# Optimization experiments

Measured on AMD Instinct MI355X. Metric: run time of the kernel, lower is better.

## Reference

```python
import jax, jax.numpy as jnp
import numpy as np

N_NODES = 50000
N_EDGES = 800000
IN_C, HID_C, OUT_C = 128, 128, 64
N_GRAPHS = 64
NEG_SLOPE = 0.2


def setup_inputs() -> dict:
    key = jax.random.key(0)
    ks = jax.random.split(key, 16)
    x = jax.random.normal(ks[0], (N_NODES, IN_C), dtype=jnp.float32)
    edge_index = jax.random.randint(ks[1], (2, N_EDGES), 0, N_NODES, dtype=jnp.int64)
    batch = jnp.sort(jax.random.randint(ks[2], (N_NODES,), 0, N_GRAPHS, dtype=jnp.int64))
    dims = [(IN_C, HID_C), (HID_C, HID_C), (HID_C, OUT_C)]
    inp = {"x": x, "edge_index": edge_index, "batch": batch}
    for l, (din, dout) in enumerate(dims):
        s = 1.0 / np.sqrt(din)
        inp[f"W{l}"] = jax.random.normal(ks[3 + 4 * l], (din, dout), dtype=jnp.float32) * s
        inp[f"as{l}"] = jax.random.normal(ks[4 + 4 * l], (dout,), dtype=jnp.float32) * 0.1
        inp[f"ad{l}"] = jax.random.normal(ks[5 + 4 * l], (dout,), dtype=jnp.float32) * 0.1
        inp[f"b{l}"] = jnp.zeros((dout,), dtype=jnp.float32)
    return inp


def gat_conv(x, src, dst, W, a_src, a_dst, b, n_nodes):
    # h: [N, dout]
    h = x @ W
    alpha_src = h @ a_src  # [N]
    alpha_dst = h @ a_dst  # [N]
    logits = jax.nn.leaky_relu(alpha_src[src] + alpha_dst[dst], NEG_SLOPE)  # [E]
    # segment softmax over incoming edges of each dst node
    m = jax.ops.segment_max(logits, dst, num_segments=n_nodes)
    e = jnp.exp(logits - m[dst])
    denom = jax.ops.segment_sum(e, dst, num_segments=n_nodes)
    alpha = e / denom[dst]  # [E]
    out = jax.ops.segment_sum(alpha[:, None] * h[src], dst, num_segments=n_nodes)
    return out + b


def reference(x, edge_index, batch, W0, as0, ad0, b0, W1, as1, ad1, b1, W2, as2, ad2, b2):
    n = x.shape[0]
    # add self loops (PyG GATConv default)
    loop = jnp.arange(n, dtype=edge_index.dtype)
    src = jnp.concatenate([edge_index[0], loop])
    dst = jnp.concatenate([edge_index[1], loop])
    h = jax.nn.relu(gat_conv(x, src, dst, W0, as0, ad0, b0, n))
    h = jax.nn.relu(gat_conv(h, src, dst, W1, as1, ad1, b1, n))
    h = gat_conv(h, src, dst, W2, as2, ad2, b2, n)
    # global_add_pool
    return jax.ops.segment_sum(h, batch, num_segments=N_GRAPHS)
```

## Files before the change

kernel.cpp:

```cpp
#include <hip/hip_runtime.h>
#include <hip/hip_fp16.h>
#include <math.h>

#define N_NODES 50000
#define N_EDGES 800000
#define N_GRAPHS 64
#define NEG_SLOPE 0.2f
#define SLOTS 64

#define BIN_NODES 256
#define NBINS 196
#define CAP 6144
#define P1_BLOCKS 192
#define BATCH 2048

__device__ __forceinline__ float leaky(float x) {
    return x > 0.f ? x : NEG_SLOPE * x;
}

struct __align__(8) half4 {
    __half2 a, b;
};

template <int DOUT>
__device__ __forceinline__ void gemm_body(const float* __restrict__ X,
                                          const float* __restrict__ W,
                                          const float* __restrict__ a_src,
                                          const float* __restrict__ a_dst,
                                          half4* __restrict__ H,
                                          float* __restrict__ as_,
                                          float* __restrict__ ad_, int N, int bid,
                                          float* xsmem) {
    constexpr int DIN = 128;
    constexpr int CG = DOUT / 4;
    constexpr int RG = 256 / CG;
    constexpr int TILE_N = RG * 4;
    float (*xs)[DIN] = reinterpret_cast<float (*)[DIN]>(xsmem);

    const int n0 = bid * TILE_N;
    const int tid = threadIdx.x;

    for (int idx = tid; idx < TILE_N * (DIN / 4); idx += 256) {
        int r = idx / (DIN / 4);
        int q = idx % (DIN / 4);
        int n = n0 + r;
        float4 v = make_float4(0.f, 0.f, 0.f, 0.f);
        if (n < N) v = reinterpret_cast<const float4*>(X)[n * (DIN / 4) + q];
        reinterpret_cast<float4*>(&xs[r][0])[q] = v;
    }
    __syncthreads();

    const int cg = tid % CG;
    const int rg = tid / CG;
    const int c0 = cg * 4;
    const int r0 = rg * 4;

    float acc[4][4] = {};
    for (int k = 0; k < DIN; k += 4) {
        float4 w[4];
#pragma unroll
        for (int kk = 0; kk < 4; ++kk)
            w[kk] = *reinterpret_cast<const float4*>(&W[(k + kk) * DOUT + c0]);
#pragma unroll
        for (int i = 0; i < 4; ++i) {
            float4 xv = *reinterpret_cast<const float4*>(&xs[r0 + i][k]);
            const float xk[4] = {xv.x, xv.y, xv.z, xv.w};
#pragma unroll
            for (int kk = 0; kk < 4; ++kk) {
                acc[i][0] += xk[kk] * w[kk].x;
                acc[i][1] += xk[kk] * w[kk].y;
                acc[i][2] += xk[kk] * w[kk].z;
                acc[i][3] += xk[kk] * w[kk].w;
            }
        }
    }

    const float4 asv = *reinterpret_cast<const float4*>(&a_src[c0]);
    const float4 adv = *reinterpret_cast<const float4*>(&a_dst[c0]);
#pragma unroll
    for (int i = 0; i < 4; ++i) {
        const int n = n0 + r0 + i;
        if (n < N) {
            half4 o;
            o.a = __floats2half2_rn(acc[i][0], acc[i][1]);
            o.b = __floats2half2_rn(acc[i][2], acc[i][3]);
            H[(size_t)n * CG + cg] = o;
        }
        float ps = acc[i][0] * asv.x + acc[i][1] * asv.y + acc[i][2] * asv.z + acc[i][3] * asv.w;
        float pd = acc[i][0] * adv.x + acc[i][1] * adv.y + acc[i][2] * adv.z + acc[i][3] * adv.w;
#pragma unroll
        for (int off = CG / 2; off; off >>= 1) {
            ps += __shfl_xor(ps, off, 64);
            pd += __shfl_xor(pd, off, 64);
        }
        if (cg == 0 && n < N) {
            as_[n] = ps;
            ad_[n] = pd;
        }
    }
}

template <int DOUT>
__global__ __launch_bounds__(256) void gemm_kernel(const float* __restrict__ X,
                                                   const float* __restrict__ W,
                                                   const float* __restrict__ a_src,
                                                   const float* __restrict__ a_dst,
                                                   half4* __restrict__ H,
                                                   float* __restrict__ as_,
                                                   float* __restrict__ ad_, int N) {
    constexpr int TILE_N = (256 / (DOUT / 4)) * 4;
    __shared__ __align__(16) float xs[TILE_N][128];
    gemm_body<DOUT>(X, W, a_src, a_dst, H, as_, ad_, N, blockIdx.x, &xs[0][0]);
}

struct P1Smem {
    unsigned int stage[BATCH];
    int hist[NBINS];
    int off[NBINS];
    unsigned int gbase[NBINS];
    int total;
};

__device__ __forceinline__ void fill_pass1(const int* __restrict__ src,
                                           const int* __restrict__ dst,
                                           unsigned int* __restrict__ bin_cursor,
                                           unsigned int* __restrict__ bin_buf,
                                           int E, int bid, void* smem_raw) {
    P1Smem& S = *reinterpret_cast<P1Smem*>(smem_raw);
    const int tid = threadIdx.x;
    const int nbatch = (E + BATCH - 1) / BATCH;
    for (int b = bid; b < nbatch; b += P1_BLOCKS) {
        __syncthreads();
        for (int i = tid; i < NBINS; i += 256) S.hist[i] = 0;
        const int e0 = b * BATCH;
        unsigned int pk[8];
        int rk[8];
        bool ok[8];
#pragma unroll
        for (int k = 0; k < 8; ++k) {
            int e = e0 + tid + k * 256;
            ok[k] = (e < E);
            int d = ok[k] ? dst[e] : 0;
            int s = ok[k] ? src[e] : 0;
            pk[k] = ((unsigned)d << 16) | (unsigned)s;
            rk[k] = 0;
        }
        __syncthreads();
#pragma unroll
        for (int k = 0; k < 8; ++k)
            if (ok[k]) rk[k] = atomicAdd(&S.hist[pk[k] >> 24], 1);
        __syncthreads();
        if (tid == 0) {
            int run = 0;
            for (int i = 0; i < NBINS; ++i) {
                S.off[i] = run;
                run += S.hist[i];
            }
            S.total = run;
        }
        __syncthreads();
        if (tid < NBINS && S.hist[tid] > 0)
            S.gbase[tid] = atomicAdd(&bin_cursor[tid], (unsigned)S.hist[tid]);
#pragma unroll
        for (int k = 0; k < 8; ++k)
            if (ok[k]) S.stage[S.off[pk[k] >> 24] + rk[k]] = pk[k];
        __syncthreads();
        const int tot = S.total;
        for (int i = tid; i < tot; i += 256) {
            unsigned int v = S.stage[i];
            int bn = v >> 24;
            unsigned int p = S.gbase[bn] + (unsigned)(i - S.off[bn]);
            if (p < CAP) bin_buf[(size_t)bn * CAP + p] = v;
        }
    }
}

__global__ __launch_bounds__(256) void gemm0_fill_kernel(
    const float* __restrict__ X, const float* __restrict__ W,
    const float* __restrict__ a_src, const float* __restrict__ a_dst,
    half4* __restrict__ H, float* __restrict__ as_, float* __restrict__ ad_, int N,
    const int* __restrict__ src, const int* __restrict__ dst,
    unsigned int* __restrict__ bin_cursor, unsigned int* __restrict__ bin_buf, int E) {
    __shared__ __align__(16) unsigned char smem[16384];
    if (blockIdx.x < P1_BLOCKS) {
        fill_pass1(src, dst, bin_cursor, bin_buf, E, blockIdx.x, smem);
        return;
    }
    gemm_body<128>(X, W, a_src, a_dst, H, as_, ad_, N, blockIdx.x - P1_BLOCKS,
                   reinterpret_cast<float*>(smem));
}

__global__ __launch_bounds__(256) void fill_pass2(const unsigned int* __restrict__ bin_cursor,
                                                  const unsigned int* __restrict__ bin_buf,
                                                  int* __restrict__ cursor,
                                                  unsigned short* __restrict__ col, int N) {
    __shared__ unsigned short bk[BIN_NODES][SLOTS];
    __shared__ int cnt[BIN_NODES];
    const int b = blockIdx.x;
    const int tid = threadIdx.x;
    const int base = b * BIN_NODES;
    const int nn = min(BIN_NODES, N - base);
    if (nn <= 0) return;
    cnt[tid] = 0;
    __syncthreads();
    const int ec = min((int)bin_cursor[b], CAP);
    for (int i = tid; i < ec; i += 256) {
        unsigned int v = bin_buf[(size_t)b * CAP + i];
        int d = (int)(v >> 16) - base;
        int p = atomicAdd(&cnt[d], 1);
        if (p < SLOTS) bk[d][p] = (unsigned short)(v & 0xFFFFu);
    }
    __syncthreads();
    unsigned int* col32 = reinterpret_cast<unsigned int*>(col);
    const unsigned int* lds32 = reinterpret_cast<const unsigned int*>(&bk[0][0]);
    const int words = nn * (SLOTS / 2);
    for (int i = tid; i < words; i += 256)
        col32[(size_t)base * (SLOTS / 2) + i] = lds32[i];
    if (tid < nn) cursor[base + tid] = cnt[tid];
}

template <int DOUT, bool RELU>
__global__ __launch_bounds__(256) void gather_kernel(const half4* __restrict__ H,
                                                     const float* __restrict__ as_,
                                                     const float* __restrict__ ad_,
                                                     const int* __restrict__ cursor,
                                                     const unsigned short* __restrict__ col,
                                                     const float* __restrict__ bias,
                                                     float* __restrict__ OUT, int N) {
    constexpr int NCH4 = DOUT / 4;
    constexpr int SUBS = 64 / NCH4;
    const int node = blockIdx.x * 4 + (threadIdx.x >> 6);
    if (node >= N) return;
    const int l = threadIdx.x & 63;
    const int ch = l & (NCH4 - 1);
    const int sub = l / NCH4;

    const float adn = ad_[node];
    const float sl = leaky(as_[node] + adn);
    const int rs = node << 6;
    const int re = rs + min(cursor[node], SLOTS);

    float4 acc = make_float4(0.f, 0.f, 0.f, 0.f);
    float dsum = 0.f;

    int i = rs + sub;
    for (; i + 7 * SUBS < re; i += 8 * SUBS) {
        int s[8];
        float a[8];
        half4 h[8];
#pragma unroll
        for (int u = 0; u < 8; ++u) s[u] = col[i + u * SUBS];
#pragma unroll
        for (int u = 0; u < 8; ++u) a[u] = as_[s[u]];
#pragma unroll
        for (int u = 0; u < 8; ++u) h[u] = H[(size_t)s[u] * NCH4 + ch];
#pragma unroll
        for (int u = 0; u < 8; ++u) {
            float ee = __expf(leaky(a[u] + adn));
            float2 f0 = __half22float2(h[u].a);
            float2 f1 = __half22float2(h[u].b);
            acc.x += ee * f0.x;
            acc.y += ee * f0.y;
            acc.z += ee * f1.x;
            acc.w += ee * f1.y;
            dsum += ee;
        }
    }
    for (; i + 3 * SUBS < re; i += 4 * SUBS) {
        int s[4];
        float a[4];
        half4 h[4];
#pragma unroll
        for (int u = 0; u < 4; ++u) s[u] = col[i + u * SUBS];
#pragma unroll
        for (int u = 0; u < 4; ++u) a[u] = as_[s[u]];
#pragma unroll
        for (int u = 0; u < 4; ++u) h[u] = H[(size_t)s[u] * NCH4 + ch];
#pragma unroll
        for (int u = 0; u < 4; ++u) {
            float ee = __expf(leaky(a[u] + adn));
            float2 f0 = __half22float2(h[u].a);
            float2 f1 = __half22float2(h[u].b);
            acc.x += ee * f0.x;
            acc.y += ee * f0.y;
            acc.z += ee * f1.x;
            acc.w += ee * f1.y;
            dsum += ee;
        }
    }
    for (; i < re; i += SUBS) {
        int s0 = col[i];
        float e0 = __expf(leaky(as_[s0] + adn));
        half4 h0 = H[(size_t)s0 * NCH4 + ch];
        float2 f0 = __half22float2(h0.a);
        float2 f1 = __half22float2(h0.b);
        acc.x += e0 * f0.x;
        acc.y += e0 * f0.y;
        acc.z += e0 * f1.x;
        acc.w += e0 * f1.y;
        dsum += e0;
    }

#pragma unroll
    for (int off = 32; off >= NCH4; off >>= 1)
        dsum += __shfl_xor(dsum, off, 64);
#pragma unroll
    for (int off = 32; off >= NCH4; off >>= 1) {
        acc.x += __shfl_down(acc.x, off, 64);
        acc.y += __shfl_down(acc.y, off, 64);
        acc.z += __shfl_down(acc.z, off, 64);
        acc.w += __shfl_down(acc.w, off, 64);
    }

    if (l < NCH4) {
        const float e_self = __expf(sl);
        half4 h = H[(size_t)node * NCH4 + ch];
        float2 f0 = __half22float2(h.a);
        float2 f1 = __half22float2(h.b);
        acc.x += e_self * f0.x;
        acc.y += e_self * f0.y;
        acc.z += e_self * f1.x;
        acc.w += e_self * f1.y;
        const float inv = 1.f / (dsum + e_self);
        const float4 b4 = reinterpret_cast<const float4*>(bias)[ch];
        float4 r;
        r.x = acc.x * inv + b4.x;
        r.y = acc.y * inv + b4.y;
        r.z = acc.z * inv + b4.z;
        r.w = acc.w * inv + b4.w;
        if (RELU) {
            r.x = fmaxf(r.x, 0.f);
            r.y = fmaxf(r.y, 0.f);
            r.z = fmaxf(r.z, 0.f);
            r.w = fmaxf(r.w, 0.f);
        }
        reinterpret_cast<float4*>(OUT)[(size_t)node * NCH4 + ch] = r;
    }
}

__global__ __launch_bounds__(256) void pool_kernel(const float* __restrict__ H2,
                                                   const int* __restrict__ batch,
                                                   float* __restrict__ out, int N) {
    const int wv = threadIdx.x >> 6;
    const int c = threadIdx.x & 63;
    const int n0 = blockIdx.x * 128 + wv * 32;
    if (n0 >= N) return;
    const int n1 = min(n0 + 32, N);
    float acc = 0.f;
    int cur = batch[n0];
    for (int n = n0; n < n1; ++n) {
        int g = batch[n];
        if (g != cur) {
            atomicAdd(&out[cur * 64 + c], acc);
            acc = 0.f;
            cur = g;
        }
        acc += H2[n * 64 + c];
    }
    atomicAdd(&out[cur * 64 + c], acc);
}

extern "C" void kernel_launch(void* const* d_in, const int* in_sizes, int n_in,
                              void* d_out, int out_size, void* d_ws, size_t ws_size,
                              hipStream_t stream) {
    const float* x = (const float*)d_in[0];
    const int* edge_index = (const int*)d_in[1];
    const int* batch = (const int*)d_in[2];
    const float* W0 = (const float*)d_in[3];
    const float* as0 = (const float*)d_in[4];
    const float* ad0 = (const float*)d_in[5];
    const float* b0 = (const float*)d_in[6];
    const float* W1 = (const float*)d_in[7];
    const float* as1 = (const float*)d_in[8];
    const float* ad1 = (const float*)d_in[9];
    const float* b1 = (const float*)d_in[10];
    const float* W2 = (const float*)d_in[11];
    const float* as2 = (const float*)d_in[12];
    const float* ad2 = (const float*)d_in[13];
    const float* b2 = (const float*)d_in[14];

    const int* e_src = edge_index;
    const int* e_dst = edge_index + N_EDGES;

    float* B0 = (float*)d_ws;
    half4* H = (half4*)(B0 + N_NODES * 128);
    float* as_ = (float*)H + N_NODES * 128;
    float* ad_ = as_ + N_NODES;
    int* cursor = (int*)(ad_ + N_NODES);
    unsigned short* col = (unsigned short*)(cursor + N_NODES);
    unsigned int* bin_cursor = (unsigned int*)(col + (size_t)N_NODES * SLOTS);
    unsigned int* bin_buf = bin_cursor + NBINS;

    hipMemsetAsync(bin_cursor, 0, NBINS * sizeof(unsigned int), stream);

    const int NODE_BLOCKS = (N_NODES + 3) / 4;
    const int GEMM128_BLOCKS = (N_NODES + 31) / 32;

    gemm0_fill_kernel<<<P1_BLOCKS + GEMM128_BLOCKS, 256, 0, stream>>>(
        x, W0, as0, ad0, H, as_, ad_, N_NODES, e_src, e_dst, bin_cursor, bin_buf, N_EDGES);
    fill_pass2<<<NBINS, 256, 0, stream>>>(bin_cursor, bin_buf, cursor, col, N_NODES);
    gather_kernel<128, true><<<NODE_BLOCKS, 256, 0, stream>>>(H, as_, ad_, cursor, col, b0, B0, N_NODES);

    gemm_kernel<128><<<GEMM128_BLOCKS, 256, 0, stream>>>(B0, W1, as1, ad1, H, as_, ad_, N_NODES);
    gather_kernel<128, true><<<NODE_BLOCKS, 256, 0, stream>>>(H, as_, ad_, cursor, col, b1, B0, N_NODES);

    gemm_kernel<64><<<(N_NODES + 63) / 64, 256, 0, stream>>>(B0, W2, as2, ad2, H, as_, ad_, N_NODES);
    gather_kernel<64, false><<<NODE_BLOCKS, 256, 0, stream>>>(H, as_, ad_, cursor, col, b2, B0, N_NODES);

    hipMemsetAsync(d_out, 0, (size_t)out_size * sizeof(float), stream);
    pool_kernel<<<(N_NODES + 127) / 128, 256, 0, stream>>>(B0, batch, (float*)d_out, N_NODES);
}
```

Before: 311.6 us.

## Replace FP32 scalar GEMMs with FP16 MFMA using pre-swizzled weight tiles

Replaces the per-layer scalar FP32 GEMM (x@W plus attention projections) with a 16x16x32 FP16 MFMA kernel. Inputs are converted to half and stored in a swizzled LDS tile, and the weights are pre-packed into the MFMA operand layout by a new prep kernel. That prep kernel also zeroes the bin cursors, replacing a memset call. This is meant to move the dense projection work onto matrix cores. In exchange it adds an extra launch and rounds the inputs to FP16, which lowers precision before accumulation.

New measurement: 267.6 us. -14.1%, faster.

```diff
diff --git a/kernel.cpp b/kernel.cpp
--- a/kernel.cpp
+++ b/kernel.cpp
@@ -14,6 +14,9 @@
 #define P1_BLOCKS 192
 #define BATCH 2048
 
+typedef _Float16 f16x8 __attribute__((ext_vector_type(8)));
+typedef float f32x4 __attribute__((ext_vector_type(4)));
+
 __device__ __forceinline__ float leaky(float x) {
     return x > 0.f ? x : NEG_SLOPE * x;
 }
@@ -22,95 +25,131 @@
     __half2 a, b;
 };
 
+__global__ __launch_bounds__(256) void prep_kernel(const float* __restrict__ W0,
+                                                   const float* __restrict__ W1,
+                                                   const float* __restrict__ W2,
+                                                   _Float16* __restrict__ Wt0,
+                                                   _Float16* __restrict__ Wt1,
+                                                   _Float16* __restrict__ Wt2,
+                                                   unsigned int* __restrict__ bin_cursor) {
+    const int t = blockIdx.x * 256 + threadIdx.x;
+    if (t < NBINS) bin_cursor[t] = 0;
+    const float* W;
+    _Float16* Wt;
+    int g, CTl, DOUTl;
+    if (t < 2048) { W = W0; Wt = Wt0; g = t; CTl = 8; DOUTl = 128; }
+    else if (t < 4096) { W = W1; Wt = Wt1; g = t - 2048; CTl = 8; DOUTl = 128; }
+    else if (t < 5120) { W = W2; Wt = Wt2; g = t - 4096; CTl = 4; DOUTl = 64; }
+    else return;
+    const int kt = g / (CTl * 64);
+    const int rem = g % (CTl * 64);
+    const int ct = rem / 64;
+    const int lane = rem % 64;
+    const int kbase = kt * 32 + (lane >> 4) * 8;
+    const int c = ct * 16 + (lane & 15);
+#pragma unroll
+    for (int b = 0; b < 8; ++b)
+        Wt[(size_t)g * 8 + b] = (_Float16)W[(size_t)(kbase + b) * DOUTl + c];
+}
+
 template <int DOUT>
-__device__ __forceinline__ void gemm_body(const float* __restrict__ X,
-                                          const float* __restrict__ W,
-                                          const float* __restrict__ a_src,
-                                          const float* __restrict__ a_dst,
-                                          half4* __restrict__ H,
-                                          float* __restrict__ as_,
-                                          float* __restrict__ ad_, int N, int bid,
-                                          float* xsmem) {
-    constexpr int DIN = 128;
-    constexpr int CG = DOUT / 4;
-    constexpr int RG = 256 / CG;
-    constexpr int TILE_N = RG * 4;
-    float (*xs)[DIN] = reinterpret_cast<float (*)[DIN]>(xsmem);
-
-    const int n0 = bid * TILE_N;
+__device__ __forceinline__ void mfma_gemm_body(const float* __restrict__ X,
+                                               const _Float16* __restrict__ Wt,
+                                               const float* __restrict__ a_src,
+                                               const float* __restrict__ a_dst,
+                                               _Float16* __restrict__ H,
+                                               float* __restrict__ as_,
+                                               float* __restrict__ ad_, int N, int bid,
+                                               _Float16* xs) {
+    constexpr int CT = DOUT / 16;
     const int tid = threadIdx.x;
-
-    for (int idx = tid; idx < TILE_N * (DIN / 4); idx += 256) {
-        int r = idx / (DIN / 4);
-        int q = idx % (DIN / 4);
-        int n = n0 + r;
-        float4 v = make_float4(0.f, 0.f, 0.f, 0.f);
-        if (n < N) v = reinterpret_cast<const float4*>(X)[n * (DIN / 4) + q];
-        reinterpret_cast<float4*>(&xs[r][0])[q] = v;
+    const int n0 = bid * 64;
+    const float4* X4 = reinterpret_cast<const float4*>(X);
+
+    for (int idx = tid; idx < 64 * 16; idx += 256) {
+        const int r = idx >> 4, q = idx & 15;
+        const int n = n0 + r;
+        float4 v0 = make_float4(0.f, 0.f, 0.f, 0.f), v1 = v0;
+        if (n < N) {
+            v0 = X4[(size_t)n * 32 + 2 * q];
+            v1 = X4[(size_t)n * 32 + 2 * q + 1];
+        }
+        f16x8 hv;
+        hv[0] = (_Float16)v0.x; hv[1] = (_Float16)v0.y;
+        hv[2] = (_Float16)v0.z; hv[3] = (_Float16)v0.w;
+        hv[4] = (_Float16)v1.x; hv[5] = (_Float16)v1.y;
+        hv[6] = (_Float16)v1.z; hv[7] = (_Float16)v1.w;
+        *reinterpret_cast<f16x8*>(&xs[r * 128 + ((q ^ (r & 15)) << 3)]) = hv;
     }
     __syncthreads();
 
-    const int cg = tid % CG;
-    const int rg = tid / CG;
-    const int c0 = cg * 4;
-    const int r0 = rg * 4;
-
-    float acc[4][4] = {};
-    for (int k = 0; k < DIN; k += 4) {
-        float4 w[4];
-#pragma unroll
-        for (int kk = 0; kk < 4; ++kk)
-            w[kk] = *reinterpret_cast<const float4*>(&W[(k + kk) * DOUT + c0]);
-#pragma unroll
-        for (int i = 0; i < 4; ++i) {
-            float4 xv = *reinterpret_cast<const float4*>(&xs[r0 + i][k]);
-            const float xk[4] = {xv.x, xv.y, xv.z, xv.w};
-#pragma unroll
-            for (int kk = 0; kk < 4; ++kk) {
-                acc[i][0] += xk[kk] * w[kk].x;
-                acc[i][1] += xk[kk] * w[kk].y;
-                acc[i][2] += xk[kk] * w[kk].z;
-                acc[i][3] += xk[kk] * w[kk].w;
+    const int wave = tid >> 6, lane = tid & 63;
+    const int colb = lane & 15;
+    const int kg = lane >> 4;
+    const int arow = wave * 16 + colb;
+
+    f32x4 acc[CT];
+#pragma unroll
+    for (int ct = 0; ct < CT; ++ct) {
+        acc[ct][0] = 0.f; acc[ct][1] = 0.f; acc[ct][2] = 0.f; acc[ct][3] = 0.f;
+    }
+    const f16x8* Wt8 = reinterpret_cast<const f16x8*>(Wt);
+#pragma unroll
+    for (int kt = 0; kt < 4; ++kt) {
+        f16x8 A = *reinterpret_cast<const f16x8*>(
+            &xs[arow * 128 + (((kt * 4 + kg) ^ (arow & 15)) << 3)]);
+#pragma unroll
+        for (int ct = 0; ct < CT; ++ct) {
+            f16x8 B = Wt8[(kt * CT + ct) * 64 + lane];
+            acc[ct] = __builtin_amdgcn_mfma_f32_16x16x32_f16(A, B, acc[ct], 0, 0, 0);
+        }
+    }
+
+    float ps[4] = {0.f, 0.f, 0.f, 0.f}, pd[4] = {0.f, 0.f, 0.f, 0.f};
+#pragma unroll
+    for (int ct = 0; ct < CT; ++ct) {
+        const int col = ct * 16 + colb;
+        const float asv = a_src[col];
+        const float adv = a_dst[col];
+#pragma unroll
+        for (int r = 0; r < 4; ++r) {
+            const float d = acc[ct][r];
+            ps[r] += d * asv;
+            pd[r] += d * adv;
+            const int row = n0 + wave * 16 + kg * 4 + r;
+            if (row < N) H[(size_t)row * DOUT + col] = (_Float16)d;
+        }
+    }
+#pragma unroll
+    for (int off = 1; off < 16; off <<= 1) {
+#pragma unroll
+        for (int r = 0; r < 4; ++r) {
+            ps[r] += __shfl_xor(ps[r], off, 64);
+            pd[r] += __shfl_xor(pd[r], off, 64);
+        }
+    }
+    if (colb == 0) {
+#pragma unroll
+        for (int r = 0; r < 4; ++r) {
+            const int row = n0 + wave * 16 + kg * 4 + r;
+            if (row < N) {
+                as_[row] = ps[r];
+                ad_[row] = pd[r];
             }
         }
     }
-
-    const float4 asv = *reinterpret_cast<const float4*>(&a_src[c0]);
-    const float4 adv = *reinterpret_cast<const float4*>(&a_dst[c0]);
-#pragma unroll
-    for (int i = 0; i < 4; ++i) {
-        const int n = n0 + r0 + i;
-        if (n < N) {
-            half4 o;
-            o.a = __floats2half2_rn(acc[i][0], acc[i][1]);
-            o.b = __floats2half2_rn(acc[i][2], acc[i][3]);
-            H[(size_t)n * CG + cg] = o;
-        }
-        float ps = acc[i][0] * asv.x + acc[i][1] * asv.y + acc[i][2] * asv.z + acc[i][3] * asv.w;
-        float pd = acc[i][0] * adv.x + acc[i][1] * adv.y + acc[i][2] * adv.z + acc[i][3] * adv.w;
-#pragma unroll
-        for (int off = CG / 2; off; off >>= 1) {
-            ps += __shfl_xor(ps, off, 64);
-            pd += __shfl_xor(pd, off, 64);
-        }
-        if (cg == 0 && n < N) {
-            as_[n] = ps;
-            ad_[n] = pd;
-        }
-    }
 }
 
 template <int DOUT>
-__global__ __launch_bounds__(256) void gemm_kernel(const float* __restrict__ X,
-                                                   const float* __restrict__ W,
-                                                   const float* __restrict__ a_src,
-                                                   const float* __restrict__ a_dst,
-                                                   half4* __restrict__ H,
-                                                   float* __restrict__ as_,
-                                                   float* __restrict__ ad_, int N) {
-    constexpr int TILE_N = (256 / (DOUT / 4)) * 4;
-    __shared__ __align__(16) float xs[TILE_N][128];
-    gemm_body<DOUT>(X, W, a_src, a_dst, H, as_, ad_, N, blockIdx.x, &xs[0][0]);
+__global__ __launch_bounds__(256) void mfma_gemm_kernel(const float* __restrict__ X,
+                                                        const _Float16* __restrict__ Wt,
+                                                        const float* __restrict__ a_src,
+                                                        const float* __restrict__ a_dst,
+                                                        _Float16* __restrict__ H,
+                                                        float* __restrict__ as_,
+                                                        float* __restrict__ ad_, int N) {
+    __shared__ __align__(16) _Float16 xs[64 * 128];
+    mfma_gemm_body<DOUT>(X, Wt, a_src, a_dst, H, as_, ad_, N, blockIdx.x, xs);
 }
 
 struct P1Smem {
@@ -176,9 +215,9 @@
 }
 
 __global__ __launch_bounds__(256) void gemm0_fill_kernel(
-    const float* __restrict__ X, const float* __restrict__ W,
+    const float* __restrict__ X, const _Float16* __restrict__ Wt0,
     const float* __restrict__ a_src, const float* __restrict__ a_dst,
-    half4* __restrict__ H, float* __restrict__ as_, float* __restrict__ ad_, int N,
+    _Float16* __restrict__ H, float* __restrict__ as_, float* __restrict__ ad_, int N,
     const int* __restrict__ src, const int* __restrict__ dst,
     unsigned int* __restrict__ bin_cursor, unsigned int* __restrict__ bin_buf, int E) {
     __shared__ __align__(16) unsigned char smem[16384];
@@ -186,8 +225,8 @@
         fill_pass1(src, dst, bin_cursor, bin_buf, E, blockIdx.x, smem);
         return;
     }
-    gemm_body<128>(X, W, a_src, a_dst, H, as_, ad_, N, blockIdx.x - P1_BLOCKS,
-                   reinterpret_cast<float*>(smem));
+    mfma_gemm_body<128>(X, Wt0, a_src, a_dst, H, as_, ad_, N, blockIdx.x - P1_BLOCKS,
+                        reinterpret_cast<_Float16*>(smem));
 }
 
 __global__ __launch_bounds__(256) void fill_pass2(const unsigned int* __restrict__ bin_cursor,
@@ -382,30 +421,37 @@
     const int* e_src = edge_index;
     const int* e_dst = edge_index + N_EDGES;
 
-    float* B0 = (float*)d_ws;
-    half4* H = (half4*)(B0 + N_NODES * 128);
-    float* as_ = (float*)H + N_NODES * 128;
-    float* ad_ = as_ + N_NODES;
-    int* cursor = (int*)(ad_ + N_NODES);
-    unsigned short* col = (unsigned short*)(cursor + N_NODES);
-    unsigned int* bin_cursor = (unsigned int*)(col + (size_t)N_NODES * SLOTS);
-    unsigned int* bin_buf = bin_cursor + NBINS;
-
-    hipMemsetAsync(bin_cursor, 0, NBINS * sizeof(unsigned int), stream);
+    char* p = (char*)d_ws;
+    float* B0 = (float*)p;            p += (size_t)N_NODES * 128 * 4;
+    _Float16* H = (_Float16*)p;       p += (size_t)N_NODES * 128 * 2;
+    float* as_ = (float*)p;           p += (size_t)N_NODES * 4;
+    float* ad_ = (float*)p;           p += (size_t)N_NODES * 4;
+    int* cursor = (int*)p;            p += (size_t)N_NODES * 4;
+    unsigned short* col = (unsigned short*)p; p += (size_t)N_NODES * SLOTS * 2;
+    unsigned int* bin_cursor = (unsigned int*)p; p += (size_t)NBINS * 4;
+    unsigned int* bin_buf = (unsigned int*)p; p += (size_t)NBINS * CAP * 4;
+    _Float16* Wt0 = (_Float16*)p;     p += (size_t)16384 * 2;
+    _Float16* Wt1 = (_Float16*)p;     p += (size_t)16384 * 2;
+    _Float16* Wt2 = (_Float16*)p;     p += (size_t)8192 * 2;
 
     const int NODE_BLOCKS = (N_NODES + 3) / 4;
-    const int GEMM128_BLOCKS = (N_NODES + 31) / 32;
-
-    gemm0_fill_kernel<<<P1_BLOCKS + GEMM128_BLOCKS, 256, 0, stream>>>(
-        x, W0, as0, ad0, H, as_, ad_, N_NODES, e_src, e_dst, bin_cursor, bin_buf, N_EDGES);
+    const int GEMM_BLOCKS = (N_NODES + 63) / 64;
+
+    prep_kernel<<<20, 256, 0, stream>>>(W0, W1, W2, Wt0, Wt1, Wt2, bin_cursor);
+
+    gemm0_fill_kernel<<<P1_BLOCKS + GEMM_BLOCKS, 256, 0, stream>>>(
+        x, Wt0, as0, ad0, H, as_, ad_, N_NODES, e_src, e_dst, bin_cursor, bin_buf, N_EDGES);
     fill_pass2<<<NBINS, 256, 0, stream>>>(bin_cursor, bin_buf, cursor, col, N_NODES);
-    gather_kernel<128, true><<<NODE_BLOCKS, 256, 0, stream>>>(H, as_, ad_, cursor, col, b0, B0, N_NODES);
-
-    gemm_kernel<128><<<GEMM128_BLOCKS, 256, 0, stream>>>(B0, W1, as1, ad1, H, as_, ad_, N_NODES);
-    gather_kernel<128, true><<<NODE_BLOCKS, 256, 0, stream>>>(H, as_, ad_, cursor, col, b1, B0, N_NODES);
-
-    gemm_kernel<64><<<(N_NODES + 63) / 64, 256, 0, stream>>>(B0, W2, as2, ad2, H, as_, ad_, N_NODES);
-    gather_kernel<64, false><<<NODE_BLOCKS, 256, 0, stream>>>(H, as_, ad_, cursor, col, b2, B0, N_NODES);
+    gather_kernel<128, true><<<NODE_BLOCKS, 256, 0, stream>>>(
+        (const half4*)H, as_, ad_, cursor, col, b0, B0, N_NODES);
+
+    mfma_gemm_kernel<128><<<GEMM_BLOCKS, 256, 0, stream>>>(B0, Wt1, as1, ad1, H, as_, ad_, N_NODES);
+    gather_kernel<128, true><<<NODE_BLOCKS, 256, 0, stream>>>(
+        (const half4*)H, as_, ad_, cursor, col, b1, B0, N_NODES);
+
+    mfma_gemm_kernel<64><<<GEMM_BLOCKS, 256, 0, stream>>>(B0, Wt2, as2, ad2, H, as_, ad_, N_NODES);
+    gather_kernel<64, false><<<NODE_BLOCKS, 256, 0, stream>>>(
+        (const half4*)H, as_, ad_, cursor, col, b2, B0, N_NODES);
 
     hipMemsetAsync(d_out, 0, (size_t)out_size * sizeof(float), stream);
     pool_kernel<<<(N_NODES + 127) / 128, 256, 0, stream>>>(B0, batch, (float*)d_out, N_NODES);
```
